# Kernel optimization log

Hardware: AMD Instinct MI355X
Metric: run time of the kernel (lower is better)

Reference implementation:

```python
import jax, jax.numpy as jnp
import numpy as np

THRESH = 0.6
MIN_KEPT = 200000
FACTOR = 8
IGNORE_LABEL = -1


def _lin_coords(n_in, n_out):
    # scipy.ndimage.zoom (grid_mode=False): input_coord = i * (n_in-1)/(n_out-1)
    return jnp.linspace(0.0, n_in - 1.0, n_out)


def _zoom_bilinear(x, h_out, w_out):
    # x: (n, c, h, w) -> (n, c, h_out, w_out), separable order-1 (bilinear) zoom
    h, w = x.shape[-2], x.shape[-1]
    yc = _lin_coords(h, h_out)
    xc = _lin_coords(w, w_out)
    y0 = jnp.floor(yc).astype(jnp.int32)
    y1 = jnp.minimum(y0 + 1, h - 1)
    wy = (yc - y0)[None, None, :, None]
    x0 = jnp.floor(xc).astype(jnp.int32)
    x1 = jnp.minimum(x0 + 1, w - 1)
    wx = xc - x0
    a = jnp.take(x, y0, axis=2) * (1.0 - wy) + jnp.take(x, y1, axis=2) * wy
    return jnp.take(a, x0, axis=3) * (1.0 - wx) + jnp.take(a, x1, axis=3) * wx


def _zoom_nearest(t, h_out, w_out):
    # t: (n, h, w) int labels -> (n, h_out, w_out), order-0 (nearest) zoom
    h, w = t.shape[-2], t.shape[-1]
    yi = jnp.round(_lin_coords(h, h_out)).astype(jnp.int32)
    xi = jnp.round(_lin_coords(w, w_out)).astype(jnp.int32)
    return t[:, yi][:, :, xi]


def setup_inputs() -> dict:
    key = jax.random.key(0)
    k1, k2 = jax.random.split(key)
    predict = jax.random.normal(k1, (8, 19, 512, 1024), dtype=jnp.float32)
    target = jax.random.randint(k2, (8, 512, 1024), 0, 19, dtype=jnp.int32)
    return {"predict": predict, "target": target}


def reference(predict, target):
    n, c, h, w = predict.shape
    prob = jax.nn.softmax(predict, axis=1)  # (n, c, h, w)

    # ---- find_threshold: quantile on the factor-downsampled prediction ----
    h_s, w_s = int(round(h / FACTOR)), int(round(w / FACTOR))
    prob_s = _zoom_bilinear(prob, h_s, w_s)          # (n, c, h_s, w_s)
    tgt_s = _zoom_nearest(target, h_s, w_s)          # (n, h_s, w_s)
    # pred_s[i] = prob_s[n_i, label_i, y_i, x_i]
    pred_s = jnp.take_along_axis(prob_s, tgt_s[:, None].astype(jnp.int32), axis=1)[:, 0].ravel()
    min_kept_s = MIN_KEPT // (FACTOR * FACTOR)
    k_th = min(int(pred_s.shape[0]), min_kept_s) - 1  # static
    kth_val = jnp.sort(pred_s)[k_th]                  # == np.partition(pred, k_th)[k_th]
    threshold = jnp.where(kth_val > THRESH, kth_val, jnp.float32(THRESH))

    # ---- generate_new_target: keep hard pixels (pred prob <= threshold) ----
    pred_full = jnp.take_along_axis(prob, target[:, None].astype(jnp.int32), axis=1)[:, 0]  # (n, h, w)
    kept = (pred_full <= threshold) & (target >= 0)
    new_target = jnp.where(kept, target, IGNORE_LABEL)
    return new_target
```

## Files before the change

kernel.cpp:

```cpp
#include <hip/hip_runtime.h>
#include <math.h>

#define N_IMG 8
#define C_CH 19
#define H_IMG 512
#define W_IMG 1024
#define HW (H_IMG * W_IMG)
#define HS 64
#define WSDS 128
#define NDS (N_IMG * HS * WSDS)
#define K_TH 3124
#define THRESH_F 0.6f

typedef float  f32x4 __attribute__((ext_vector_type(4)));
typedef int    i32x4 __attribute__((ext_vector_type(4)));

__global__ __launch_bounds__(256) void k1_pred_s(const float* __restrict__ predict,
                                                 const int* __restrict__ target,
                                                 float* __restrict__ pred_s) {
    int t = threadIdx.x;
    int g = blockIdx.x * 64 + (t >> 2);
    int cr = t & 3;
    int n = g >> 13;
    int r = g & 8191;
    int j = r >> 7;
    int i = r & 127;

    float yc = (float)j * (511.0f / 63.0f);
    float xc = (float)i * (1023.0f / 127.0f);
    int y0 = (int)floorf(yc);
    if (y0 > H_IMG - 1) y0 = H_IMG - 1;
    int y1 = min(y0 + 1, H_IMG - 1);
    float wy = yc - (float)y0;
    int x0 = (int)floorf(xc);
    if (x0 > W_IMG - 1) x0 = W_IMG - 1;
    int x1 = min(x0 + 1, W_IMG - 1);
    float wx = xc - (float)x0;

    int yi = min((int)rintf(yc), H_IMG - 1);
    int xi = min((int)rintf(xc), W_IMG - 1);
    int L = target[n * HW + yi * W_IMG + xi];
    if (L < 0) L = 0;

    int yy = (cr & 2) ? y1 : y0;
    int xx = (cr & 1) ? x1 : x0;
    float w = ((cr & 2) ? wy : 1.0f - wy) * ((cr & 1) ? wx : 1.0f - wx);

    const float* pp = predict + (size_t)n * C_CH * HW + yy * W_IMG + xx;
    float v[C_CH];
    float m = -INFINITY;
    #pragma unroll
    for (int c = 0; c < C_CH; c++) {
        float x = pp[(size_t)c * HW];
        v[c] = x;
        m = fmaxf(m, x);
    }
    float s = 0.0f, eL = 0.0f;
    #pragma unroll
    for (int c = 0; c < C_CH; c++) {
        float e = expf(v[c] - m);
        s += e;
        if (c == L) eL = e;
    }
    float p = w * (eL / s);

    p += __shfl_xor(p, 1, 64);
    p += __shfl_xor(p, 2, 64);
    if (cr == 0) pred_s[g] = p;
}

#define K2_THREADS 1024
#define K2_WAVES (K2_THREADS / 64)

__global__ __launch_bounds__(K2_THREADS) void k2_select(const float* __restrict__ pred_s,
                                                        float* __restrict__ thr_out) {
    __shared__ unsigned int hist[K2_WAVES * 2048];
    __shared__ unsigned int tot[2048];
    __shared__ unsigned int wsum[K2_WAVES];
    __shared__ unsigned int s_bin, s_k;

    const int t = threadIdx.x;
    const int lane = t & 63;
    const int wave = t >> 6;

    unsigned int prefix = 0;
    unsigned int k = K_TH;

    for (int lvl = 0; lvl < 3; lvl++) {
        const int nb = (lvl == 2) ? 1024 : 2048;

        for (int b = t; b < K2_WAVES * nb; b += K2_THREADS) hist[b] = 0;
        __syncthreads();

        unsigned int* myhist = &hist[wave * nb];
        for (int idx = t; idx < NDS; idx += K2_THREADS) {
            unsigned int u = __float_as_uint(pred_s[idx]);
            bool ok;
            unsigned int bin;
            if (lvl == 0)      { ok = true;                bin = u >> 21; }
            else if (lvl == 1) { ok = (u >> 21) == prefix; bin = (u >> 10) & 2047u; }
            else               { ok = (u >> 10) == prefix; bin = u & 1023u; }
            if (ok) atomicAdd(&myhist[bin], 1u);
        }
        __syncthreads();

        for (int b = t; b < nb; b += K2_THREADS) {
            unsigned int s = 0;
            #pragma unroll
            for (int w = 0; w < K2_WAVES; w++) s += hist[w * nb + b];
            tot[b] = s;
        }
        __syncthreads();

        unsigned int c0, c1, s;
        if (nb == 2048) { c0 = tot[2 * t]; c1 = tot[2 * t + 1]; s = c0 + c1; }
        else            { c0 = tot[t];     c1 = 0;              s = c0; }

        unsigned int incl = s;
        #pragma unroll
        for (int off = 1; off < 64; off <<= 1) {
            unsigned int v = (unsigned int)__shfl_up((int)incl, off, 64);
            if (lane >= off) incl += v;
        }
        if (lane == 63) wsum[wave] = incl;
        __syncthreads();
        unsigned int woff = 0;
        for (int w = 0; w < wave; w++) woff += wsum[w];
        unsigned int excl = woff + incl - s;

        if (k >= excl && k < excl + s) {
            if (nb == 2048) {
                if (k < excl + c0) { s_bin = 2u * t;     s_k = k - excl; }
                else               { s_bin = 2u * t + 1; s_k = k - excl - c0; }
            } else {
                s_bin = (unsigned int)t; s_k = k - excl;
            }
        }
        __syncthreads();

        unsigned int b = s_bin;
        k = s_k;
        if (lvl == 0)      prefix = b;
        else if (lvl == 1) prefix = (prefix << 11) | b;
        else               prefix = (prefix << 10) | b;
        __syncthreads();
    }

    if (t == 0) {
        float kth = __uint_as_float(prefix);
        *thr_out = (kth > THRESH_F) ? kth : THRESH_F;
    }
}

__global__ __launch_bounds__(256) void k3_final(const float* __restrict__ predict,
                                                const int* __restrict__ target,
                                                const float* __restrict__ thr_ptr,
                                                int* __restrict__ out) {
    int tid = blockIdx.x * blockDim.x + threadIdx.x;
    int p = tid * 4;
    if (p >= N_IMG * HW) return;
    int n = p >> 19;
    int o = p & (HW - 1);
    const float* base = predict + (size_t)n * C_CH * HW + o;

    i32x4 tg = *reinterpret_cast<const i32x4*>(target + p);

    f32x4 v[C_CH];
    f32x4 m = (f32x4)(-INFINITY);
    #pragma unroll
    for (int c = 0; c < C_CH; c++) {
        f32x4 x = __builtin_nontemporal_load(
            reinterpret_cast<const f32x4*>(base + (size_t)c * HW));
        v[c] = x;
        m.x = fmaxf(m.x, x.x); m.y = fmaxf(m.y, x.y);
        m.z = fmaxf(m.z, x.z); m.w = fmaxf(m.w, x.w);
    }
    f32x4 s = (f32x4)(0.0f);
    f32x4 et = (f32x4)(0.0f);
    #pragma unroll
    for (int c = 0; c < C_CH; c++) {
        float ex = expf(v[c].x - m.x);
        float ey = expf(v[c].y - m.y);
        float ez = expf(v[c].z - m.z);
        float ew = expf(v[c].w - m.w);
        s.x += ex; s.y += ey; s.z += ez; s.w += ew;
        if (c == tg.x) et.x = ex;
        if (c == tg.y) et.y = ey;
        if (c == tg.z) et.z = ez;
        if (c == tg.w) et.w = ew;
    }
    float thr = *thr_ptr;
    i32x4 r;
    r.x = ((et.x / s.x) <= thr && tg.x >= 0) ? tg.x : -1;
    r.y = ((et.y / s.y) <= thr && tg.y >= 0) ? tg.y : -1;
    r.z = ((et.z / s.z) <= thr && tg.z >= 0) ? tg.z : -1;
    r.w = ((et.w / s.w) <= thr && tg.w >= 0) ? tg.w : -1;
    __builtin_nontemporal_store(r, reinterpret_cast<i32x4*>(out + p));
}

extern "C" void kernel_launch(void* const* d_in, const int* in_sizes, int n_in,
                              void* d_out, int out_size, void* d_ws, size_t ws_size,
                              hipStream_t stream) {
    const float* predict = (const float*)d_in[0];
    const int* target    = (const int*)d_in[1];
    int* out = (int*)d_out;

    float* pred_s = (float*)d_out;
    float* thr    = (float*)d_ws;

    hipLaunchKernelGGL(k1_pred_s, dim3(NDS * 4 / 256), dim3(256), 0, stream,
                       predict, target, pred_s);
    hipLaunchKernelGGL(k2_select, dim3(1), dim3(K2_THREADS), 0, stream, pred_s, thr);
    hipLaunchKernelGGL(k3_final, dim3((N_IMG * HW) / (4 * 256)), dim3(256), 0, stream,
                       predict, target, thr, out);
}
```

Measured before the change: 474.4 us.

## Fuse downsampled-prob scatter into full softmax pass and cache per-pixel target prob

The full-resolution softmax pass now also writes each pixel's target-class probability to a workspace buffer. Pixels that are bilinear corners of the downsampled grid scatter their weighted contributions into pred_s with atomics, which replaces the separate k1 gather kernel. The final mask kernel then reads only the cached probability and the target instead of recomputing softmax over 19 channels. This trades a second 159 MB predict read for a 16 MB write plus re-read, a zeroing launch, float atomics whose summation order is nondeterministic, and extra per-pixel index arithmetic.

```diff
diff --git a/kernel.cpp b/kernel.cpp
--- a/kernel.cpp
+++ b/kernel.cpp
@@ -6,161 +6,28 @@
 #define H_IMG 512
 #define W_IMG 1024
 #define HW (H_IMG * W_IMG)
-#define HS 64
-#define WSDS 128
-#define NDS (N_IMG * HS * WSDS)
+#define NDS (N_IMG * 64 * 128)
 #define K_TH 3124
 #define THRESH_F 0.6f
 
 typedef float  f32x4 __attribute__((ext_vector_type(4)));
 typedef int    i32x4 __attribute__((ext_vector_type(4)));
 
-__global__ __launch_bounds__(256) void k1_pred_s(const float* __restrict__ predict,
-                                                 const int* __restrict__ target,
-                                                 float* __restrict__ pred_s) {
-    int t = threadIdx.x;
-    int g = blockIdx.x * 64 + (t >> 2);
-    int cr = t & 3;
-    int n = g >> 13;
-    int r = g & 8191;
-    int j = r >> 7;
-    int i = r & 127;
-
-    float yc = (float)j * (511.0f / 63.0f);
-    float xc = (float)i * (1023.0f / 127.0f);
-    int y0 = (int)floorf(yc);
-    if (y0 > H_IMG - 1) y0 = H_IMG - 1;
-    int y1 = min(y0 + 1, H_IMG - 1);
-    float wy = yc - (float)y0;
-    int x0 = (int)floorf(xc);
-    if (x0 > W_IMG - 1) x0 = W_IMG - 1;
-    int x1 = min(x0 + 1, W_IMG - 1);
-    float wx = xc - (float)x0;
-
-    int yi = min((int)rintf(yc), H_IMG - 1);
-    int xi = min((int)rintf(xc), W_IMG - 1);
-    int L = target[n * HW + yi * W_IMG + xi];
-    if (L < 0) L = 0;
-
-    int yy = (cr & 2) ? y1 : y0;
-    int xx = (cr & 1) ? x1 : x0;
-    float w = ((cr & 2) ? wy : 1.0f - wy) * ((cr & 1) ? wx : 1.0f - wx);
-
-    const float* pp = predict + (size_t)n * C_CH * HW + yy * W_IMG + xx;
-    float v[C_CH];
-    float m = -INFINITY;
-    #pragma unroll
-    for (int c = 0; c < C_CH; c++) {
-        float x = pp[(size_t)c * HW];
-        v[c] = x;
-        m = fmaxf(m, x);
-    }
-    float s = 0.0f, eL = 0.0f;
-    #pragma unroll
-    for (int c = 0; c < C_CH; c++) {
-        float e = expf(v[c] - m);
-        s += e;
-        if (c == L) eL = e;
-    }
-    float p = w * (eL / s);
-
-    p += __shfl_xor(p, 1, 64);
-    p += __shfl_xor(p, 2, 64);
-    if (cr == 0) pred_s[g] = p;
-}
-
-#define K2_THREADS 1024
-#define K2_WAVES (K2_THREADS / 64)
-
-__global__ __launch_bounds__(K2_THREADS) void k2_select(const float* __restrict__ pred_s,
-                                                        float* __restrict__ thr_out) {
-    __shared__ unsigned int hist[K2_WAVES * 2048];
-    __shared__ unsigned int tot[2048];
-    __shared__ unsigned int wsum[K2_WAVES];
-    __shared__ unsigned int s_bin, s_k;
-
-    const int t = threadIdx.x;
-    const int lane = t & 63;
-    const int wave = t >> 6;
-
-    unsigned int prefix = 0;
-    unsigned int k = K_TH;
-
-    for (int lvl = 0; lvl < 3; lvl++) {
-        const int nb = (lvl == 2) ? 1024 : 2048;
-
-        for (int b = t; b < K2_WAVES * nb; b += K2_THREADS) hist[b] = 0;
-        __syncthreads();
-
-        unsigned int* myhist = &hist[wave * nb];
-        for (int idx = t; idx < NDS; idx += K2_THREADS) {
-            unsigned int u = __float_as_uint(pred_s[idx]);
-            bool ok;
-            unsigned int bin;
-            if (lvl == 0)      { ok = true;                bin = u >> 21; }
-            else if (lvl == 1) { ok = (u >> 21) == prefix; bin = (u >> 10) & 2047u; }
-            else               { ok = (u >> 10) == prefix; bin = u & 1023u; }
-            if (ok) atomicAdd(&myhist[bin], 1u);
-        }
-        __syncthreads();
-
-        for (int b = t; b < nb; b += K2_THREADS) {
-            unsigned int s = 0;
-            #pragma unroll
-            for (int w = 0; w < K2_WAVES; w++) s += hist[w * nb + b];
-            tot[b] = s;
-        }
-        __syncthreads();
-
-        unsigned int c0, c1, s;
-        if (nb == 2048) { c0 = tot[2 * t]; c1 = tot[2 * t + 1]; s = c0 + c1; }
-        else            { c0 = tot[t];     c1 = 0;              s = c0; }
-
-        unsigned int incl = s;
-        #pragma unroll
-        for (int off = 1; off < 64; off <<= 1) {
-            unsigned int v = (unsigned int)__shfl_up((int)incl, off, 64);
-            if (lane >= off) incl += v;
-        }
-        if (lane == 63) wsum[wave] = incl;
-        __syncthreads();
-        unsigned int woff = 0;
-        for (int w = 0; w < wave; w++) woff += wsum[w];
-        unsigned int excl = woff + incl - s;
-
-        if (k >= excl && k < excl + s) {
-            if (nb == 2048) {
-                if (k < excl + c0) { s_bin = 2u * t;     s_k = k - excl; }
-                else               { s_bin = 2u * t + 1; s_k = k - excl - c0; }
-            } else {
-                s_bin = (unsigned int)t; s_k = k - excl;
-            }
-        }
-        __syncthreads();
-
-        unsigned int b = s_bin;
-        k = s_k;
-        if (lvl == 0)      prefix = b;
-        else if (lvl == 1) prefix = (prefix << 11) | b;
-        else               prefix = (prefix << 10) | b;
-        __syncthreads();
-    }
-
-    if (t == 0) {
-        float kth = __uint_as_float(prefix);
-        *thr_out = (kth > THRESH_F) ? kth : THRESH_F;
-    }
-}
-
-__global__ __launch_bounds__(256) void k3_final(const float* __restrict__ predict,
+__global__ __launch_bounds__(256) void k0_zero(float* __restrict__ pred_s) {
+    int idx = (blockIdx.x * 256 + threadIdx.x) * 4;
+    *reinterpret_cast<f32x4*>(pred_s + idx) = (f32x4)(0.0f);
+}
+
+__global__ __launch_bounds__(256) void k1_fused(const float* __restrict__ predict,
                                                 const int* __restrict__ target,
-                                                const float* __restrict__ thr_ptr,
-                                                int* __restrict__ out) {
+                                                float* __restrict__ pred_full,
+                                                float* __restrict__ pred_s) {
     int tid = blockIdx.x * blockDim.x + threadIdx.x;
     int p = tid * 4;
-    if (p >= N_IMG * HW) return;
     int n = p >> 19;
     int o = p & (HW - 1);
+    int y = o >> 10;
+    int xb = o & 1023;
     const float* base = predict + (size_t)n * C_CH * HW + o;
 
     i32x4 tg = *reinterpret_cast<const i32x4*>(target + p);
@@ -189,12 +56,157 @@
         if (c == tg.z) et.z = ez;
         if (c == tg.w) et.w = ew;
     }
+    f32x4 pf;
+    pf.x = et.x / s.x; pf.y = et.y / s.y; pf.z = et.z / s.z; pf.w = et.w / s.w;
+    *reinterpret_cast<f32x4*>(pred_full + p) = pf;
+
+    int jm[2]; float wym[2]; int yrow[2]; int nym = 0;
+    {
+        int jc = (int)((float)y * (63.0f / 511.0f));
+        for (int dj = -1; dj <= 2; dj++) {
+            int j = jc + dj;
+            if (j < 0 || j > 63) continue;
+            float yc = (float)j * (511.0f / 63.0f);
+            int y0 = (int)yc;
+            if (y0 > H_IMG - 1) y0 = H_IMG - 1;
+            int y1 = min(y0 + 1, H_IMG - 1);
+            float wy = yc - (float)y0;
+            int yi = min((int)rintf(yc), H_IMG - 1);
+            if (y0 == y && nym < 2) { jm[nym] = j; wym[nym] = 1.0f - wy; yrow[nym] = yi; nym++; }
+            if (y1 == y && nym < 2) { jm[nym] = j; wym[nym] = wy;        yrow[nym] = yi; nym++; }
+        }
+    }
+    if (nym) {
+        #pragma unroll
+        for (int k = 0; k < 4; k++) {
+            int x = xb + k;
+            int im[2]; float wxm[2]; int xcol[2]; int nxm = 0;
+            int ic = (int)((float)x * (127.0f / 1023.0f));
+            for (int di = -1; di <= 2; di++) {
+                int i = ic + di;
+                if (i < 0 || i > 127) continue;
+                float xc = (float)i * (1023.0f / 127.0f);
+                int x0 = (int)xc;
+                if (x0 > W_IMG - 1) x0 = W_IMG - 1;
+                int x1 = min(x0 + 1, W_IMG - 1);
+                float wx = xc - (float)x0;
+                int xi = min((int)rintf(xc), W_IMG - 1);
+                if (x0 == x && nxm < 2) { im[nxm] = i; wxm[nxm] = 1.0f - wx; xcol[nxm] = xi; nxm++; }
+                if (x1 == x && nxm < 2) { im[nxm] = i; wxm[nxm] = wx;        xcol[nxm] = xi; nxm++; }
+            }
+            for (int a = 0; a < nym; a++) {
+                for (int b = 0; b < nxm; b++) {
+                    int L = target[n * HW + yrow[a] * W_IMG + xcol[b]];
+                    if (L < 0) L = 0;
+                    float vL = v[0][k];
+                    #pragma unroll
+                    for (int c = 1; c < C_CH; c++) if (c == L) vL = v[c][k];
+                    float e = expf(vL - m[k]);
+                    float contrib = wym[a] * wxm[b] * (e / s[k]);
+                    atomicAdd(&pred_s[n * 8192 + jm[a] * 128 + im[b]], contrib);
+                }
+            }
+        }
+    }
+}
+
+#define K2_THREADS 1024
+#define K2_WAVES (K2_THREADS / 64)
+
+__global__ __launch_bounds__(K2_THREADS) void k2_select(const float* __restrict__ pred_s,
+                                                        float* __restrict__ thr_out) {
+    __shared__ unsigned int hist[K2_WAVES * 2048];
+    __shared__ unsigned int tot[2048];
+    __shared__ unsigned int wsum[K2_WAVES];
+    __shared__ unsigned int s_bin, s_k;
+
+    const int t = threadIdx.x;
+    const int lane = t & 63;
+    const int wave = t >> 6;
+
+    unsigned int prefix = 0;
+    unsigned int k = K_TH;
+
+    for (int lvl = 0; lvl < 3; lvl++) {
+        const int nb = (lvl == 2) ? 1024 : 2048;
+
+        for (int b = t; b < K2_WAVES * nb; b += K2_THREADS) hist[b] = 0;
+        __syncthreads();
+
+        unsigned int* myhist = &hist[wave * nb];
+        for (int idx = t; idx < NDS; idx += K2_THREADS) {
+            unsigned int u = __float_as_uint(pred_s[idx]);
+            bool ok;
+            unsigned int bin;
+            if (lvl == 0)      { ok = true;                bin = u >> 21; }
+            else if (lvl == 1) { ok = (u >> 21) == prefix; bin = (u >> 10) & 2047u; }
+            else               { ok = (u >> 10) == prefix; bin = u & 1023u; }
+            if (ok) atomicAdd(&myhist[bin], 1u);
+        }
+        __syncthreads();
+
+        for (int b = t; b < nb; b += K2_THREADS) {
+            unsigned int sm = 0;
+            #pragma unroll
+            for (int w = 0; w < K2_WAVES; w++) sm += hist[w * nb + b];
+            tot[b] = sm;
+        }
+        __syncthreads();
+
+        unsigned int c0, c1, s;
+        if (nb == 2048) { c0 = tot[2 * t]; c1 = tot[2 * t + 1]; s = c0 + c1; }
+        else            { c0 = tot[t];     c1 = 0;              s = c0; }
+
+        unsigned int incl = s;
+        #pragma unroll
+        for (int off = 1; off < 64; off <<= 1) {
+            unsigned int vv = (unsigned int)__shfl_up((int)incl, off, 64);
+            if (lane >= off) incl += vv;
+        }
+        if (lane == 63) wsum[wave] = incl;
+        __syncthreads();
+        unsigned int woff = 0;
+        for (int w = 0; w < wave; w++) woff += wsum[w];
+        unsigned int excl = woff + incl - s;
+
+        if (k >= excl && k < excl + s) {
+            if (nb == 2048) {
+                if (k < excl + c0) { s_bin = 2u * t;     s_k = k - excl; }
+                else               { s_bin = 2u * t + 1; s_k = k - excl - c0; }
+            } else {
+                s_bin = (unsigned int)t; s_k = k - excl;
+            }
+        }
+        __syncthreads();
+
+        unsigned int b = s_bin;
+        k = s_k;
+        if (lvl == 0)      prefix = b;
+        else if (lvl == 1) prefix = (prefix << 11) | b;
+        else               prefix = (prefix << 10) | b;
+        __syncthreads();
+    }
+
+    if (t == 0) {
+        float kth = __uint_as_float(prefix);
+        *thr_out = (kth > THRESH_F) ? kth : THRESH_F;
+    }
+}
+
+__global__ __launch_bounds__(256) void k3_mask(const float* __restrict__ pred_full,
+                                               const int* __restrict__ target,
+                                               const float* __restrict__ thr_ptr,
+                                               int* __restrict__ out) {
+    int tid = blockIdx.x * blockDim.x + threadIdx.x;
+    int p = tid * 4;
+    f32x4 pf = *reinterpret_cast<const f32x4*>(pred_full + p);
+    i32x4 tg = *reinterpret_cast<const i32x4*>(target + p);
     float thr = *thr_ptr;
     i32x4 r;
-    r.x = ((et.x / s.x) <= thr && tg.x >= 0) ? tg.x : -1;
-    r.y = ((et.y / s.y) <= thr && tg.y >= 0) ? tg.y : -1;
-    r.z = ((et.z / s.z) <= thr && tg.z >= 0) ? tg.z : -1;
-    r.w = ((et.w / s.w) <= thr && tg.w >= 0) ? tg.w : -1;
+    r.x = (pf.x <= thr && tg.x >= 0) ? tg.x : -1;
+    r.y = (pf.y <= thr && tg.y >= 0) ? tg.y : -1;
+    r.z = (pf.z <= thr && tg.z >= 0) ? tg.z : -1;
+    r.w = (pf.w <= thr && tg.w >= 0) ? tg.w : -1;
     __builtin_nontemporal_store(r, reinterpret_cast<i32x4*>(out + p));
 }
 
@@ -205,12 +217,14 @@
     const int* target    = (const int*)d_in[1];
     int* out = (int*)d_out;
 
-    float* pred_s = (float*)d_out;
-    float* thr    = (float*)d_ws;
-
-    hipLaunchKernelGGL(k1_pred_s, dim3(NDS * 4 / 256), dim3(256), 0, stream,
-                       predict, target, pred_s);
+    float* thr       = (float*)d_ws;
+    float* pred_s    = (float*)((char*)d_ws + 4096);
+    float* pred_full = (float*)((char*)d_ws + (1 << 20));
+
+    hipLaunchKernelGGL(k0_zero, dim3(NDS / (256 * 4)), dim3(256), 0, stream, pred_s);
+    hipLaunchKernelGGL(k1_fused, dim3(N_IMG * HW / (4 * 256)), dim3(256), 0, stream,
+                       predict, target, pred_full, pred_s);
     hipLaunchKernelGGL(k2_select, dim3(1), dim3(K2_THREADS), 0, stream, pred_s, thr);
-    hipLaunchKernelGGL(k3_final, dim3((N_IMG * HW) / (4 * 256)), dim3(256), 0, stream,
-                       predict, target, thr, out);
-}
+    hipLaunchKernelGGL(k3_mask, dim3(N_IMG * HW / (4 * 256)), dim3(256), 0, stream,
+                       pred_full, target, thr, out);
+}
```

Measured after the change: 471.6 us. No clear change (-0.6%).
